# Performance work log

Hardware: AMD Instinct MI355X
Metric: run time of the kernel (lower is better)

The kernel has to match this reference:

```python
import jax, jax.numpy as jnp
import numpy as np

B, C, H, W = 8, 256, 80, 80
NH, NP = 8, 4               # num_heads, num_points
CPH = C // NH               # channels per head


def conv1x1(x, w, b):
    # x: [B,Cin,H,W], w: [Cout,Cin], b: [Cout]
    return jnp.einsum('bchw,oc->bohw', x, w) + b[None, :, None, None]


def grid_sample_bilinear(img, grid):
    # img: [N,C,Hi,Wi], grid: [N,Hg,Wg,2] in [-1,1] (x,y), align_corners=True, zeros padding
    N, Cc, Hi, Wi = img.shape
    Hg, Wg = grid.shape[1], grid.shape[2]
    ix = (grid[..., 0] + 1.0) * 0.5 * (Wi - 1)
    iy = (grid[..., 1] + 1.0) * 0.5 * (Hi - 1)
    x0 = jnp.floor(ix); y0 = jnp.floor(iy)
    x1 = x0 + 1.0;      y1 = y0 + 1.0
    wx1 = ix - x0; wx0 = 1.0 - wx1
    wy1 = iy - y0; wy0 = 1.0 - wy1
    imf = img.reshape(N, Cc, Hi * Wi)

    def gather(xc, yc):
        valid = (xc >= 0) & (xc <= Wi - 1) & (yc >= 0) & (yc <= Hi - 1)
        xi = jnp.clip(xc, 0, Wi - 1).astype(jnp.int32)
        yi = jnp.clip(yc, 0, Hi - 1).astype(jnp.int32)
        idx = (yi * Wi + xi).reshape(N, 1, Hg * Wg)
        v = jnp.take_along_axis(imf, jnp.broadcast_to(idx, (N, Cc, Hg * Wg)), axis=2)
        v = v.reshape(N, Cc, Hg, Wg)
        return v * valid[:, None].astype(img.dtype)

    out = (gather(x0, y0) * (wx0 * wy0)[:, None]
           + gather(x1, y0) * (wx1 * wy0)[:, None]
           + gather(x0, y1) * (wx0 * wy1)[:, None]
           + gather(x1, y1) * (wx1 * wy1)[:, None])
    return out


def setup_inputs() -> dict:
    key = jax.random.key(0)
    ks = jax.random.split(key, 9)
    s = 1.0 / np.sqrt(C)
    x = jax.random.normal(ks[0], (B, C, H, W), dtype=jnp.float32)
    Wv = jax.random.normal(ks[1], (C, C), dtype=jnp.float32) * s
    bv = jnp.zeros((C,), dtype=jnp.float32)
    Woff = jax.random.normal(ks[2], (NH * NP * 2, C), dtype=jnp.float32) * 0.01
    boff = jax.random.normal(ks[3], (NH * NP * 2,), dtype=jnp.float32) * 0.01
    Wa = jax.random.normal(ks[4], (NH * NP, C), dtype=jnp.float32) * 0.01
    ba = jnp.full((NH * NP,), float(np.log(1.0 / NP)), dtype=jnp.float32)
    Wo = jax.random.normal(ks[5], (C, C), dtype=jnp.float32) * s
    bo = jnp.zeros((C,), dtype=jnp.float32)
    return {"x": x, "Wv": Wv, "bv": bv, "Woff": Woff, "boff": boff,
            "Wa": Wa, "ba": ba, "Wo": Wo, "bo": bo}


def reference(x, Wv, bv, Woff, boff, Wa, ba, Wo, bo):
    value = conv1x1(x, Wv, bv)                      # [B,C,H,W]
    offsets = conv1x1(x, Woff, boff)                # [B,NH*NP*2,H,W]
    attn = conv1x1(x, Wa, ba).reshape(B, NH, NP, H, W)
    attn = jax.nn.softmax(attn, axis=2)             # softmax over points

    gy, gx = jnp.meshgrid(jnp.linspace(-1.0, 1.0, H), jnp.linspace(-1.0, 1.0, W), indexing='ij')
    base_grid = jnp.stack((gx, gy), axis=-1)[None, None, None]          # [1,1,1,H,W,2]

    off = offsets.reshape(B, NH, NP, 2, H, W).transpose(0, 1, 2, 4, 5, 3)  # [B,NH,NP,H,W,2]
    grid = (base_grid + off).reshape(B * NH * NP, H, W, 2)

    v = value.reshape(B, NH, CPH, H, W)
    v = jnp.broadcast_to(v[:, :, None], (B, NH, NP, CPH, H, W)).reshape(B * NH * NP, CPH, H, W)

    sampled = grid_sample_bilinear(v, grid).reshape(B, NH, NP, CPH, H, W)
    weighted = (sampled * attn[:, :, :, None]).sum(axis=2)              # [B,NH,CPH,H,W]
    weighted = weighted.reshape(B, C, H, W)
    return conv1x1(weighted, Wo, bo) + x
```

## Files before the change

kernel.cpp:

```cpp
#include <hip/hip_runtime.h>
#include <cstddef>
#include <cstdint>

#define B_    8
#define C_    256
#define Himg  80
#define Wimg  80
#define HW_   6400
#define NH_   8
#define NP_   4
#define MPROJ 352

using bf16x8 = __attribute__((ext_vector_type(8))) short;
using f32x4  = __attribute__((ext_vector_type(4))) float;

__device__ __forceinline__ unsigned short f2bf(float f) {
    union { float f; uint32_t u; } v; v.f = f;
    uint32_t r = v.u + 0x7FFFu + ((v.u >> 16) & 1u);
    return (unsigned short)(r >> 16);
}
__device__ __forceinline__ float bf2f(unsigned short s) {
    union { uint32_t u; float f; } v; v.u = ((uint32_t)s) << 16;
    return v.f;
}

#define GLD16(gsrc, ldst) \
    __builtin_amdgcn_global_load_lds( \
        (const __attribute__((address_space(1))) unsigned int*)(gsrc), \
        (__attribute__((address_space(3))) unsigned int*)(ldst), 16, 0, 0)

__global__ __launch_bounds__(256) void prep_and_transpose(
        const float* __restrict__ Wv,  const float* __restrict__ bv,
        const float* __restrict__ Woff, const float* __restrict__ boff,
        const float* __restrict__ Wa,  const float* __restrict__ ba,
        const float* __restrict__ Wo,  const float* __restrict__ x,
        short* __restrict__ WcatBf, short* __restrict__ WoBf,
        float* __restrict__ bcat,   short* __restrict__ xT) {
    __shared__ float tile[64][68];
    const int bid = blockIdx.x;
    const int t = threadIdx.x;
    if (bid < 640) {
        int o = bid;
        if (o < 384) {
            const float* src = nullptr; float bias = 0.f;
            if (o < 256)      { src = Wv   + (size_t)o * 256;         bias = bv[o];         }
            else if (o < 320) { src = Woff + (size_t)(o - 256) * 256; bias = boff[o - 256]; }
            else if (o < 352) { src = Wa   + (size_t)(o - 320) * 256; bias = ba[o - 320];   }
            WcatBf[(size_t)o * 256 + t] = src ? (short)f2bf(src[t]) : (short)0;
            if (t == 0) bcat[o] = bias;
        } else {
            int oo = o - 384;
            WoBf[(size_t)oo * 256 + t] = (short)f2bf(Wo[(size_t)oo * 256 + t]);
        }
        return;
    }
    const int b2 = bid - 640;
    const int p0 = (b2 % 100) * 64;
    const int k0 = ((b2 / 100) & 3) * 64;
    const int b  = b2 / 400;
    const float* xb = x + ((size_t)b * C_ + k0) * HW_ + p0;
    #pragma unroll
    for (int r = 0; r < 4; ++r) {
        int kk = r * 16 + (t >> 4);
        int pp = (t & 15) * 4;
        float4 v = *(const float4*)(xb + (size_t)kk * HW_ + pp);
        *(float4*)&tile[kk][pp] = v;
    }
    __syncthreads();
    const int pp = t >> 2, kc = (t & 3) * 16;
    short tmp[16];
    #pragma unroll
    for (int i = 0; i < 16; ++i) tmp[i] = (short)f2bf(tile[kc + i][pp]);
    short* dst = xT + ((size_t)b * HW_ + p0 + pp) * 256 + k0 + kc;
    *(bf16x8*)dst       = *(bf16x8*)tmp;
    *(bf16x8*)(dst + 8) = *(bf16x8*)(tmp + 8);
}

#define PSTAGE(buf, k0)                                                         \
    _Pragma("unroll")                                                           \
    for (int q = 0; q < 4; ++q) {                                               \
        int i = wid * 4 + q;                                                    \
        int row = i * 8 + (lane >> 3);                                          \
        int sc  = (lane & 7) ^ (row & 7);                                       \
        GLD16(Wb  + (size_t)(o0 + row) * 256 + (k0) + sc * 8,                   \
              &lA[(buf)][i * 512]);                                             \
        GLD16(xTb + (size_t)(p0 + row) * 256 + (k0) + sc * 8,                   \
              &lB[(buf)][i * 512]);                                             \
    }

#define PCOMPUTE(buf)                                                           \
    _Pragma("unroll")                                                           \
    for (int kk = 0; kk < 2; ++kk) {                                            \
        bf16x8 af[4], bfr[4];                                                   \
        _Pragma("unroll")                                                       \
        for (int m = 0; m < 4; ++m) {                                           \
            int row = wo0 + m * 16 + (lane & 15);                               \
            int cph = (kk * 4 + (lane >> 4)) ^ (row & 7);                       \
            af[m] = *(const bf16x8*)&lA[(buf)][row * 64 + cph * 8];             \
        }                                                                       \
        _Pragma("unroll")                                                       \
        for (int nn = 0; nn < 4; ++nn) {                                        \
            int row = wp0 + nn * 16 + (lane & 15);                              \
            int cph = (kk * 4 + (lane >> 4)) ^ (row & 7);                       \
            bfr[nn] = *(const bf16x8*)&lB[(buf)][row * 64 + cph * 8];           \
        }                                                                       \
        _Pragma("unroll")                                                       \
        for (int m = 0; m < 4; ++m)                                             \
            _Pragma("unroll")                                                   \
            for (int nn = 0; nn < 4; ++nn)                                      \
                acc[m][nn] = __builtin_amdgcn_mfma_f32_16x16x32_bf16(           \
                    af[m], bfr[nn], acc[m][nn], 0, 0, 0);                       \
    }

__global__ __launch_bounds__(256) void gemm_proj_mfma(
        const short* __restrict__ Wb, const float* __restrict__ bcat,
        const short* __restrict__ xT,
        short* __restrict__ val, float* __restrict__ meta) {
    __shared__ short lA[2][8192];
    __shared__ short lB[2][8192];
    const int n = blockIdx.x;
    const int w = (n & 7) * 150 + (n >> 3);
    const int b = w / 150;
    const int r150 = w % 150;
    const int o0 = (r150 / 50) * 128;
    const int p0 = (r150 % 50) * 128;
    const int t = threadIdx.x;
    const int wid = t >> 6, lane = t & 63;
    const int wo0 = (wid & 1) * 64, wp0 = (wid >> 1) * 64;
    const short* xTb = xT + (size_t)b * HW_ * 256;
    f32x4 acc[4][4] = {};

    PSTAGE(0, 0)
    __syncthreads();
    #pragma unroll
    for (int kt = 0; kt < 3; ++kt) {
        const int cur = kt & 1;
        PSTAGE(cur ^ 1, (kt + 1) * 64)
        PCOMPUTE(cur)
        __syncthreads();
    }
    PCOMPUTE(1)

    #pragma unroll
    for (int m = 0; m < 4; ++m) {
        int oc = o0 + wo0 + m * 16 + (lane >> 4) * 4;
        if (oc >= MPROJ) continue;
        float4 bias = *(const float4*)(bcat + oc);
        #pragma unroll
        for (int nn = 0; nn < 4; ++nn) {
            int p = p0 + wp0 + nn * 16 + (lane & 15);
            f32x4 a = acc[m][nn];
            float v0 = a[0] + bias.x, v1 = a[1] + bias.y;
            float v2 = a[2] + bias.z, v3 = a[3] + bias.w;
            if (oc < 256) {
                int h = oc >> 5, c0 = oc & 31;
                ushort4 u;
                u.x = f2bf(v0); u.y = f2bf(v1); u.z = f2bf(v2); u.w = f2bf(v3);
                *(ushort4*)(val + (((size_t)(b * NH_ + h) * HW_) + p) * 32 + c0) = u;
            } else if (oc < 320) {
                float4 f;
                f.x = v0 * 39.5f; f.y = v1 * 39.5f;
                f.z = v2 * 39.5f; f.w = v3 * 39.5f;
                *(float4*)(meta + ((size_t)b * HW_ + p) * 96 + (oc - 256)) = f;
            } else {
                float mx = fmaxf(fmaxf(v0, v1), fmaxf(v2, v3));
                float e0 = __expf(v0 - mx), e1 = __expf(v1 - mx);
                float e2 = __expf(v2 - mx), e3 = __expf(v3 - mx);
                float inv = 1.f / (e0 + e1 + e2 + e3);
                float4 f;
                f.x = e0 * inv; f.y = e1 * inv; f.z = e2 * inv; f.w = e3 * inv;
                *(float4*)(meta + ((size_t)b * HW_ + p) * 96 + (oc - 256)) = f;
            }
        }
    }
}

__global__ __launch_bounds__(256) void sample_kern(
        const short* __restrict__ val, const float* __restrict__ meta,
        short* __restrict__ wout) {
    const int t = threadIdx.x;
    const int wid = t >> 6, lane = t & 63;
    const int sub = lane >> 5, li = lane & 31;
    const int h = li >> 2, j = li & 3;
    const int orig = blockIdx.x;
    const int b = orig & 7;
    const int p = (orig >> 3) * 8 + wid * 2 + sub;
    const int yy = p / Wimg;
    const int xx = p - yy * Wimg;

    const float* mrow = meta + ((size_t)b * HW_ + p) * 96;
    float4 wv = *(const float4*)(mrow + 64 + h * 4);
    float wgt[4] = {wv.x, wv.y, wv.z, wv.w};

    float4 offA = *(const float4*)(mrow + h * 8);
    float4 offB = *(const float4*)(mrow + h * 8 + 4);
    float ox[4] = {offA.x, offA.z, offB.x, offB.z};
    float oy[4] = {offA.y, offA.w, offB.y, offB.w};

    const short* vb = val + ((size_t)(b * NH_ + h) * HW_) * 32 + j * 8;

    float acc[8] = {};
    #pragma unroll
    for (int pt = 0; pt < NP_; ++pt) {
        float ix = (float)xx + ox[pt];
        float iy = (float)yy + oy[pt];
        float x0f = floorf(ix), y0f = floorf(iy);
        int   x0  = (int)x0f,   y0  = (int)y0f;
        float wx1 = ix - x0f, wx0 = 1.f - wx1;
        float wy1 = iy - y0f, wy0 = 1.f - wy1;
        int x0c = min(max(x0, 0), Wimg - 1), x1c = min(max(x0 + 1, 0), Wimg - 1);
        int y0c = min(max(y0, 0), Himg - 1), y1c = min(max(y0 + 1, 0), Himg - 1);
        float vx0 = (x0 >= 0 && x0 <= Wimg - 1)         ? wx0 : 0.f;
        float vx1 = (x0 + 1 >= 0 && x0 + 1 <= Wimg - 1) ? wx1 : 0.f;
        float vy0 = (y0 >= 0 && y0 <= Himg - 1)         ? wy0 : 0.f;
        float vy1 = (y0 + 1 >= 0 && y0 + 1 <= Himg - 1) ? wy1 : 0.f;
        bf16x8 u00 = *(const bf16x8*)(vb + (size_t)(y0c * Wimg + x0c) * 32);
        bf16x8 u01 = *(const bf16x8*)(vb + (size_t)(y0c * Wimg + x1c) * 32);
        bf16x8 u10 = *(const bf16x8*)(vb + (size_t)(y1c * Wimg + x0c) * 32);
        bf16x8 u11 = *(const bf16x8*)(vb + (size_t)(y1c * Wimg + x1c) * 32);
        float w00 = vy0 * vx0 * wgt[pt], w01 = vy0 * vx1 * wgt[pt];
        float w10 = vy1 * vx0 * wgt[pt], w11 = vy1 * vx1 * wgt[pt];
        #pragma unroll
        for (int c = 0; c < 8; ++c) {
            acc[c] += w00 * bf2f((unsigned short)u00[c])
                    + w01 * bf2f((unsigned short)u01[c])
                    + w10 * bf2f((unsigned short)u10[c])
                    + w11 * bf2f((unsigned short)u11[c]);
        }
    }
    short tmp[8];
    #pragma unroll
    for (int c = 0; c < 8; ++c) tmp[c] = (short)f2bf(acc[c]);
    *(bf16x8*)(wout + ((size_t)b * HW_ + p) * 256 + h * 32 + j * 8) = *(bf16x8*)tmp;
}

#define OSTAGE(buf, k0)                                                         \
    _Pragma("unroll")                                                           \
    for (int q = 0; q < 2; ++q) {                                               \
        int i = wid * 2 + q;                                                    \
        int row = i * 8 + (lane >> 3);                                          \
        int sc  = (lane & 7) ^ (row & 7);                                       \
        GLD16(Wb + (size_t)(o0 + row) * 256 + (k0) + sc * 8,                    \
              &lA[(buf)][i * 512]);                                             \
    }                                                                           \
    _Pragma("unroll")                                                           \
    for (int q = 0; q < 4; ++q) {                                               \
        int i = wid * 4 + q;                                                    \
        int row = i * 8 + (lane >> 3);                                          \
        int sc  = (lane & 7) ^ (row & 7);                                       \
        GLD16(wgtb + (size_t)(p0 + row) * 256 + (k0) + sc * 8,                  \
              &lB[(buf)][i * 512]);                                             \
    }

#define OCOMPUTE(buf)                                                           \
    _Pragma("unroll")                                                           \
    for (int kk = 0; kk < 2; ++kk) {                                            \
        bf16x8 af[4], bfr[2];                                                   \
        _Pragma("unroll")                                                       \
        for (int m = 0; m < 4; ++m) {                                           \
            int row = m * 16 + (lane & 15);                                     \
            int cph = (kk * 4 + (lane >> 4)) ^ (row & 7);                       \
            af[m] = *(const bf16x8*)&lA[(buf)][row * 64 + cph * 8];             \
        }                                                                       \
        _Pragma("unroll")                                                       \
        for (int nn = 0; nn < 2; ++nn) {                                        \
            int row = wid * 32 + nn * 16 + (lane & 15);                         \
            int cph = (kk * 4 + (lane >> 4)) ^ (row & 7);                       \
            bfr[nn] = *(const bf16x8*)&lB[(buf)][row * 64 + cph * 8];           \
        }                                                                       \
        _Pragma("unroll")                                                       \
        for (int m = 0; m < 4; ++m)                                             \
            _Pragma("unroll")                                                   \
            for (int nn = 0; nn < 2; ++nn)                                      \
                acc[m][nn] = __builtin_amdgcn_mfma_f32_16x16x32_bf16(           \
                    af[m], bfr[nn], acc[m][nn], 0, 0, 0);                       \
    }

__global__ __launch_bounds__(256) void gemm_out_mfma(
        const short* __restrict__ Wb, const float* __restrict__ bo,
        const short* __restrict__ wgt, const float* __restrict__ x,
        float* __restrict__ out) {
    __shared__ short lA[2][4096];
    __shared__ short lB[2][8192];
    const int n = blockIdx.x;
    const int w = (n & 7) * 200 + (n >> 3);
    const int b = w / 200;
    const int r200 = w % 200;
    const int o0 = (r200 / 50) * 64;
    const int p0 = (r200 % 50) * 128;
    const int t = threadIdx.x;
    const int wid = t >> 6, lane = t & 63;
    const short* wgtb = wgt + (size_t)b * HW_ * 256;
    f32x4 acc[4][2] = {};

    OSTAGE(0, 0)
    __syncthreads();
    #pragma unroll
    for (int kt = 0; kt < 3; ++kt) {
        const int cur = kt & 1;
        OSTAGE(cur ^ 1, (kt + 1) * 64)
        OCOMPUTE(cur)
        __syncthreads();
    }
    OCOMPUTE(1)

    #pragma unroll
    for (int m = 0; m < 4; ++m) {
        int oc = o0 + m * 16 + (lane >> 4) * 4;
        float4 bias = *(const float4*)(bo + oc);
        float br[4] = {bias.x, bias.y, bias.z, bias.w};
        #pragma unroll
        for (int nn = 0; nn < 2; ++nn) {
            int p = p0 + wid * 32 + nn * 16 + (lane & 15);
            f32x4 a = acc[m][nn];
            #pragma unroll
            for (int reg = 0; reg < 4; ++reg) {
                size_t ad = ((size_t)b * C_ + oc + reg) * HW_ + p;
                out[ad] = a[reg] + br[reg] + x[ad];
            }
        }
    }
}

extern "C" void kernel_launch(void* const* d_in, const int* in_sizes, int n_in,
                              void* d_out, int out_size, void* d_ws, size_t ws_size,
                              hipStream_t stream) {
    const float* x    = (const float*)d_in[0];
    const float* Wv   = (const float*)d_in[1];
    const float* bv   = (const float*)d_in[2];
    const float* Woff = (const float*)d_in[3];
    const float* boff = (const float*)d_in[4];
    const float* Wa   = (const float*)d_in[5];
    const float* ba   = (const float*)d_in[6];
    const float* Wo   = (const float*)d_in[7];
    const float* bo   = (const float*)d_in[8];
    float* out = (float*)d_out;
    char* base = (char*)d_ws;

    short* WcatBf = (short*)(base);
    short* WoBf   = (short*)(base + 196608);
    float* bcat   = (float*)(base + 327680);
    short* xT     = (short*)(base + 329728);
    short* val    = (short*)(base + 26544128);
    float* meta   = (float*)(base + 52758528);
    short* wbuf   = (short*)(base + 72419328);

    prep_and_transpose<<<dim3(3840), dim3(256), 0, stream>>>(
        Wv, bv, Woff, boff, Wa, ba, Wo, x, WcatBf, WoBf, bcat, xT);
    gemm_proj_mfma<<<dim3(1200), dim3(256), 0, stream>>>(WcatBf, bcat, xT, val, meta);
    sample_kern<<<dim3(6400), dim3(256), 0, stream>>>(val, meta, wbuf);
    gemm_out_mfma<<<dim3(1600), dim3(256), 0, stream>>>(WoBf, bo, wbuf, x, out);
}
```

Before: 100.9 us.

## Fuse bilinear sampling into output projection GEMM via shared memory tile

Merges the deformable sampling kernel and the output 1x1-conv GEMM into one kernel. Each 512-thread block samples 64 pixels for all 8 heads (one thread per pixel-head handles all 32 channels), writes the bf16 results into a swizzled LDS tile, then runs MFMA against Wo read directly from global memory. This removes the intermediate weighted buffer round-trip through HBM and one kernel launch. In exchange, each thread issues more gather loads with 32 fp32 accumulators, which raises register pressure. The Wo operand is no longer staged or pipelined through LDS, and the grid shrinks to 800 blocks.

```diff
diff --git a/kernel.cpp b/kernel.cpp
--- a/kernel.cpp
+++ b/kernel.cpp
@@ -175,148 +175,124 @@
     }
 }
 
-__global__ __launch_bounds__(256) void sample_kern(
+__global__ __launch_bounds__(512) void sample_out_mfma(
         const short* __restrict__ val, const float* __restrict__ meta,
-        short* __restrict__ wout) {
+        const short* __restrict__ Wb, const float* __restrict__ bo,
+        const float* __restrict__ x, float* __restrict__ out) {
+    __shared__ short sbuf[64 * 256];
     const int t = threadIdx.x;
-    const int wid = t >> 6, lane = t & 63;
-    const int sub = lane >> 5, li = lane & 31;
-    const int h = li >> 2, j = li & 3;
-    const int orig = blockIdx.x;
-    const int b = orig & 7;
-    const int p = (orig >> 3) * 8 + wid * 2 + sub;
-    const int yy = p / Wimg;
-    const int xx = p - yy * Wimg;
-
-    const float* mrow = meta + ((size_t)b * HW_ + p) * 96;
-    float4 wv = *(const float4*)(mrow + 64 + h * 4);
-    float wgt[4] = {wv.x, wv.y, wv.z, wv.w};
-
-    float4 offA = *(const float4*)(mrow + h * 8);
-    float4 offB = *(const float4*)(mrow + h * 8 + 4);
-    float ox[4] = {offA.x, offA.z, offB.x, offB.z};
-    float oy[4] = {offA.y, offA.w, offB.y, offB.w};
-
-    const short* vb = val + ((size_t)(b * NH_ + h) * HW_) * 32 + j * 8;
-
-    float acc[8] = {};
-    #pragma unroll
-    for (int pt = 0; pt < NP_; ++pt) {
-        float ix = (float)xx + ox[pt];
-        float iy = (float)yy + oy[pt];
-        float x0f = floorf(ix), y0f = floorf(iy);
-        int   x0  = (int)x0f,   y0  = (int)y0f;
-        float wx1 = ix - x0f, wx0 = 1.f - wx1;
-        float wy1 = iy - y0f, wy0 = 1.f - wy1;
-        int x0c = min(max(x0, 0), Wimg - 1), x1c = min(max(x0 + 1, 0), Wimg - 1);
-        int y0c = min(max(y0, 0), Himg - 1), y1c = min(max(y0 + 1, 0), Himg - 1);
-        float vx0 = (x0 >= 0 && x0 <= Wimg - 1)         ? wx0 : 0.f;
-        float vx1 = (x0 + 1 >= 0 && x0 + 1 <= Wimg - 1) ? wx1 : 0.f;
-        float vy0 = (y0 >= 0 && y0 <= Himg - 1)         ? wy0 : 0.f;
-        float vy1 = (y0 + 1 >= 0 && y0 + 1 <= Himg - 1) ? wy1 : 0.f;
-        bf16x8 u00 = *(const bf16x8*)(vb + (size_t)(y0c * Wimg + x0c) * 32);
-        bf16x8 u01 = *(const bf16x8*)(vb + (size_t)(y0c * Wimg + x1c) * 32);
-        bf16x8 u10 = *(const bf16x8*)(vb + (size_t)(y1c * Wimg + x0c) * 32);
-        bf16x8 u11 = *(const bf16x8*)(vb + (size_t)(y1c * Wimg + x1c) * 32);
-        float w00 = vy0 * vx0 * wgt[pt], w01 = vy0 * vx1 * wgt[pt];
-        float w10 = vy1 * vx0 * wgt[pt], w11 = vy1 * vx1 * wgt[pt];
-        #pragma unroll
-        for (int c = 0; c < 8; ++c) {
-            acc[c] += w00 * bf2f((unsigned short)u00[c])
-                    + w01 * bf2f((unsigned short)u01[c])
-                    + w10 * bf2f((unsigned short)u10[c])
-                    + w11 * bf2f((unsigned short)u11[c]);
-        }
-    }
-    short tmp[8];
-    #pragma unroll
-    for (int c = 0; c < 8; ++c) tmp[c] = (short)f2bf(acc[c]);
-    *(bf16x8*)(wout + ((size_t)b * HW_ + p) * 256 + h * 32 + j * 8) = *(bf16x8*)tmp;
-}
-
-#define OSTAGE(buf, k0)                                                         \
-    _Pragma("unroll")                                                           \
-    for (int q = 0; q < 2; ++q) {                                               \
-        int i = wid * 2 + q;                                                    \
-        int row = i * 8 + (lane >> 3);                                          \
-        int sc  = (lane & 7) ^ (row & 7);                                       \
-        GLD16(Wb + (size_t)(o0 + row) * 256 + (k0) + sc * 8,                    \
-              &lA[(buf)][i * 512]);                                             \
-    }                                                                           \
-    _Pragma("unroll")                                                           \
-    for (int q = 0; q < 4; ++q) {                                               \
-        int i = wid * 4 + q;                                                    \
-        int row = i * 8 + (lane >> 3);                                          \
-        int sc  = (lane & 7) ^ (row & 7);                                       \
-        GLD16(wgtb + (size_t)(p0 + row) * 256 + (k0) + sc * 8,                  \
-              &lB[(buf)][i * 512]);                                             \
-    }
-
-#define OCOMPUTE(buf)                                                           \
-    _Pragma("unroll")                                                           \
-    for (int kk = 0; kk < 2; ++kk) {                                            \
-        bf16x8 af[4], bfr[2];                                                   \
-        _Pragma("unroll")                                                       \
-        for (int m = 0; m < 4; ++m) {                                           \
-            int row = m * 16 + (lane & 15);                                     \
-            int cph = (kk * 4 + (lane >> 4)) ^ (row & 7);                       \
-            af[m] = *(const bf16x8*)&lA[(buf)][row * 64 + cph * 8];             \
-        }                                                                       \
-        _Pragma("unroll")                                                       \
-        for (int nn = 0; nn < 2; ++nn) {                                        \
-            int row = wid * 32 + nn * 16 + (lane & 15);                         \
-            int cph = (kk * 4 + (lane >> 4)) ^ (row & 7);                       \
-            bfr[nn] = *(const bf16x8*)&lB[(buf)][row * 64 + cph * 8];           \
-        }                                                                       \
-        _Pragma("unroll")                                                       \
-        for (int m = 0; m < 4; ++m)                                             \
-            _Pragma("unroll")                                                   \
-            for (int nn = 0; nn < 2; ++nn)                                      \
-                acc[m][nn] = __builtin_amdgcn_mfma_f32_16x16x32_bf16(           \
-                    af[m], bfr[nn], acc[m][nn], 0, 0, 0);                       \
-    }
-
-__global__ __launch_bounds__(256) void gemm_out_mfma(
-        const short* __restrict__ Wb, const float* __restrict__ bo,
-        const short* __restrict__ wgt, const float* __restrict__ x,
-        float* __restrict__ out) {
-    __shared__ short lA[2][4096];
-    __shared__ short lB[2][8192];
     const int n = blockIdx.x;
-    const int w = (n & 7) * 200 + (n >> 3);
-    const int b = w / 200;
-    const int r200 = w % 200;
-    const int o0 = (r200 / 50) * 64;
-    const int p0 = (r200 % 50) * 128;
-    const int t = threadIdx.x;
-    const int wid = t >> 6, lane = t & 63;
-    const short* wgtb = wgt + (size_t)b * HW_ * 256;
-    f32x4 acc[4][2] = {};
-
-    OSTAGE(0, 0)
+    const int b  = n & 7;
+    const int p0 = (n >> 3) * 64;
+
+    {
+        const int px = t >> 3;
+        const int h  = t & 7;
+        const int p  = p0 + px;
+        const int yy = p / Wimg;
+        const int xx = p - yy * Wimg;
+
+        const float* mrow = meta + ((size_t)b * HW_ + p) * 96;
+        float4 wv = *(const float4*)(mrow + 64 + h * 4);
+        float wgt[4] = {wv.x, wv.y, wv.z, wv.w};
+        float4 offA = *(const float4*)(mrow + h * 8);
+        float4 offB = *(const float4*)(mrow + h * 8 + 4);
+        float ox[4] = {offA.x, offA.z, offB.x, offB.z};
+        float oy[4] = {offA.y, offA.w, offB.y, offB.w};
+
+        const short* vb = val + ((size_t)(b * NH_ + h) * HW_) * 32;
+
+        float acc[32] = {};
+        #pragma unroll
+        for (int pt = 0; pt < NP_; ++pt) {
+            float ix = (float)xx + ox[pt];
+            float iy = (float)yy + oy[pt];
+            float x0f = floorf(ix), y0f = floorf(iy);
+            int   x0  = (int)x0f,   y0  = (int)y0f;
+            float wx1 = ix - x0f, wx0 = 1.f - wx1;
+            float wy1 = iy - y0f, wy0 = 1.f - wy1;
+            int x0c = min(max(x0, 0), Wimg - 1), x1c = min(max(x0 + 1, 0), Wimg - 1);
+            int y0c = min(max(y0, 0), Himg - 1), y1c = min(max(y0 + 1, 0), Himg - 1);
+            float vx0 = (x0 >= 0 && x0 <= Wimg - 1)         ? wx0 : 0.f;
+            float vx1 = (x0 + 1 >= 0 && x0 + 1 <= Wimg - 1) ? wx1 : 0.f;
+            float vy0 = (y0 >= 0 && y0 <= Himg - 1)         ? wy0 : 0.f;
+            float vy1 = (y0 + 1 >= 0 && y0 + 1 <= Himg - 1) ? wy1 : 0.f;
+            float cw[4] = {vy0 * vx0 * wgt[pt], vy0 * vx1 * wgt[pt],
+                           vy1 * vx0 * wgt[pt], vy1 * vx1 * wgt[pt]};
+            const short* cp[4];
+            cp[0] = vb + (size_t)(y0c * Wimg + x0c) * 32;
+            cp[1] = vb + (size_t)(y0c * Wimg + x1c) * 32;
+            cp[2] = vb + (size_t)(y1c * Wimg + x0c) * 32;
+            cp[3] = vb + (size_t)(y1c * Wimg + x1c) * 32;
+            #pragma unroll
+            for (int cr = 0; cr < 4; ++cr) {
+                bf16x8 q0 = *(const bf16x8*)(cp[cr]);
+                bf16x8 q1 = *(const bf16x8*)(cp[cr] + 8);
+                bf16x8 q2 = *(const bf16x8*)(cp[cr] + 16);
+                bf16x8 q3 = *(const bf16x8*)(cp[cr] + 24);
+                float w = cw[cr];
+                #pragma unroll
+                for (int e = 0; e < 8; ++e) {
+                    acc[e]      += w * bf2f((unsigned short)q0[e]);
+                    acc[8 + e]  += w * bf2f((unsigned short)q1[e]);
+                    acc[16 + e] += w * bf2f((unsigned short)q2[e]);
+                    acc[24 + e] += w * bf2f((unsigned short)q3[e]);
+                }
+            }
+        }
+        #pragma unroll
+        for (int part = 0; part < 4; ++part) {
+            short tmp[8];
+            #pragma unroll
+            for (int e = 0; e < 8; ++e) tmp[e] = (short)f2bf(acc[part * 8 + e]);
+            int c = (h * 4 + part) ^ (px & 7);
+            *(bf16x8*)&sbuf[px * 256 + c * 8] = *(bf16x8*)tmp;
+        }
+    }
     __syncthreads();
-    #pragma unroll
-    for (int kt = 0; kt < 3; ++kt) {
-        const int cur = kt & 1;
-        OSTAGE(cur ^ 1, (kt + 1) * 64)
-        OCOMPUTE(cur)
-        __syncthreads();
-    }
-    OCOMPUTE(1)
-
-    #pragma unroll
-    for (int m = 0; m < 4; ++m) {
-        int oc = o0 + m * 16 + (lane >> 4) * 4;
-        float4 bias = *(const float4*)(bo + oc);
-        float br[4] = {bias.x, bias.y, bias.z, bias.w};
-        #pragma unroll
-        for (int nn = 0; nn < 2; ++nn) {
-            int p = p0 + wid * 32 + nn * 16 + (lane & 15);
-            f32x4 a = acc[m][nn];
-            #pragma unroll
-            for (int reg = 0; reg < 4; ++reg) {
-                size_t ad = ((size_t)b * C_ + oc + reg) * HW_ + p;
-                out[ad] = a[reg] + br[reg] + x[ad];
+
+    {
+        const int wid = t >> 6, lane = t & 63;
+        const int wo0 = (wid >> 1) * 64;
+        const int pw0 = (wid & 1) * 32;
+        f32x4 acc[4][2] = {};
+
+        #pragma unroll
+        for (int kc = 0; kc < 8; ++kc) {
+            bf16x8 af[4], bfr[2];
+            #pragma unroll
+            for (int m = 0; m < 4; ++m) {
+                int orow = wo0 + m * 16 + (lane & 15);
+                af[m] = *(const bf16x8*)(Wb + (size_t)orow * 256 + kc * 32 + (lane >> 4) * 8);
+            }
+            #pragma unroll
+            for (int nn = 0; nn < 2; ++nn) {
+                int prow = pw0 + nn * 16 + (lane & 15);
+                int c = (kc * 4 + (lane >> 4)) ^ (prow & 7);
+                bfr[nn] = *(const bf16x8*)&sbuf[prow * 256 + c * 8];
+            }
+            #pragma unroll
+            for (int m = 0; m < 4; ++m)
+                #pragma unroll
+                for (int nn = 0; nn < 2; ++nn)
+                    acc[m][nn] = __builtin_amdgcn_mfma_f32_16x16x32_bf16(
+                        af[m], bfr[nn], acc[m][nn], 0, 0, 0);
+        }
+
+        #pragma unroll
+        for (int m = 0; m < 4; ++m) {
+            int oc = wo0 + m * 16 + (lane >> 4) * 4;
+            float4 bias = *(const float4*)(bo + oc);
+            float br[4] = {bias.x, bias.y, bias.z, bias.w};
+            #pragma unroll
+            for (int nn = 0; nn < 2; ++nn) {
+                int p = p0 + pw0 + nn * 16 + (lane & 15);
+                f32x4 a = acc[m][nn];
+                #pragma unroll
+                for (int reg = 0; reg < 4; ++reg) {
+                    size_t ad = ((size_t)b * C_ + oc + reg) * HW_ + p;
+                    out[ad] = a[reg] + br[reg] + x[ad];
+                }
             }
         }
     }
@@ -343,11 +319,9 @@
     short* xT     = (short*)(base + 329728);
     short* val    = (short*)(base + 26544128);
     float* meta   = (float*)(base + 52758528);
-    short* wbuf   = (short*)(base + 72419328);
 
     prep_and_transpose<<<dim3(3840), dim3(256), 0, stream>>>(
         Wv, bv, Woff, boff, Wa, ba, Wo, x, WcatBf, WoBf, bcat, xT);
     gemm_proj_mfma<<<dim3(1200), dim3(256), 0, stream>>>(WcatBf, bcat, xT, val, meta);
-    sample_kern<<<dim3(6400), dim3(256), 0, stream>>>(val, meta, wbuf);
-    gemm_out_mfma<<<dim3(1600), dim3(256), 0, stream>>>(WoBf, bo, wbuf, x, out);
-}
+    sample_out_mfma<<<dim3(800), dim3(512), 0, stream>>>(val, meta, WoBf, bo, x, out);
+}
```

Measured after the change: 149.4 us. +48.1%, slower.
